# Kernel tuning notes

Measured on AMD Instinct MI355X. Metric: run time of the kernel, lower is better.

The kernel has to match this reference:

```python
import jax, jax.numpy as jnp
import numpy as np

N_NODES = 50000
N_EDGES = 600000
NFEAT = 128
HIDDEN = 64
NCLASS = 40


def sage_conv(x, src, dst, Wl, bl, Wr, num_nodes):
    # PyG SAGEConv (aggr='mean'): out = lin_l(mean_{j->i} x_j) + lin_r(x_i)
    msg = x[src]                                                  # [E, d]
    agg = jax.ops.segment_sum(msg, dst, num_segments=num_nodes)   # [N, d]
    cnt = jax.ops.segment_sum(jnp.ones((src.shape[0],), x.dtype), dst,
                              num_segments=num_nodes)             # [N]
    agg = agg / jnp.maximum(cnt, 1.0)[:, None]
    return agg @ Wl.T + bl + x @ Wr.T


def setup_inputs() -> dict:
    key = jax.random.key(0)
    ks = jax.random.split(key, 8)
    x = jax.random.normal(ks[0], (N_NODES, NFEAT), dtype=jnp.float32)
    edge_index = jax.random.randint(ks[1], (2, N_EDGES), 0, N_NODES, dtype=jnp.int64)
    def glorot(k, shape):
        lim = np.sqrt(6.0 / (shape[0] + shape[1]))
        return jax.random.uniform(k, shape, jnp.float32, -lim, lim)
    Wl1 = glorot(ks[2], (HIDDEN, NFEAT))
    bl1 = jnp.zeros((HIDDEN,), jnp.float32)
    Wr1 = glorot(ks[3], (HIDDEN, NFEAT))
    Wl2 = glorot(ks[4], (NCLASS, HIDDEN))
    bl2 = jnp.zeros((NCLASS,), jnp.float32)
    Wr2 = glorot(ks[5], (NCLASS, HIDDEN))
    return {"x": x, "edge_index": edge_index, "Wl1": Wl1, "bl1": bl1,
            "Wr1": Wr1, "Wl2": Wl2, "bl2": bl2, "Wr2": Wr2}


def reference(x, edge_index, Wl1, bl1, Wr1, Wl2, bl2, Wr2):
    src, dst = edge_index[0], edge_index[1]
    h = sage_conv(x, src, dst, Wl1, bl1, Wr1, N_NODES)   # [N, 64]
    h = jax.nn.sigmoid(h)
    out = sage_conv(h, src, dst, Wl2, bl2, Wr2, N_NODES)  # [N, nclass]
    return out
```

## Files before the change

kernel.cpp:

```cpp
#include <hip/hip_runtime.h>
#include <cmath>

#define NN 50000
#define NE 600000
#define NF 128
#define NH 64
#define NC 40

#define SCAN_TPB 512
#define SCAN_NBLK 98

#define LDSP1 65
#define LDSP2 41

__global__ __launch_bounds__(256) void k_hist(const int* __restrict__ dst,
                                              int* __restrict__ deg) {
  int i0 = blockIdx.x * blockDim.x + threadIdx.x;
  int stride = gridDim.x * blockDim.x;
  for (int e = i0; e < NE; e += stride) atomicAdd(&deg[dst[e]], 1);
}

__global__ __launch_bounds__(SCAN_TPB) void k_scan1(const int* __restrict__ deg,
                                                    int* __restrict__ blocksum) {
  __shared__ int sd[SCAN_TPB];
  int i = blockIdx.x * SCAN_TPB + threadIdx.x;
  sd[threadIdx.x] = (i < NN) ? deg[i] : 0;
  __syncthreads();
  for (int off = SCAN_TPB / 2; off > 0; off >>= 1) {
    if (threadIdx.x < off) sd[threadIdx.x] += sd[threadIdx.x + off];
    __syncthreads();
  }
  if (threadIdx.x == 0) blocksum[blockIdx.x] = sd[0];
}

__global__ __launch_bounds__(128) void k_scan2(const int* __restrict__ blocksum,
                                               int* __restrict__ blockoff) {
  __shared__ int sd[128];
  int tid = threadIdx.x;
  int v = (tid < SCAN_NBLK) ? blocksum[tid] : 0;
  sd[tid] = v;
  __syncthreads();
  for (int off = 1; off < 128; off <<= 1) {
    int t = (tid >= off) ? sd[tid - off] : 0;
    __syncthreads();
    sd[tid] += t;
    __syncthreads();
  }
  if (tid < SCAN_NBLK) blockoff[tid] = sd[tid] - v;
}

__global__ __launch_bounds__(SCAN_TPB) void k_scan3(
    const int* __restrict__ deg, const int* __restrict__ blockoff,
    int* __restrict__ rowptr, int* __restrict__ cursor) {
  __shared__ int sd[SCAN_TPB];
  int tid = threadIdx.x;
  int i = blockIdx.x * SCAN_TPB + tid;
  int v = (i < NN) ? deg[i] : 0;
  sd[tid] = v;
  __syncthreads();
  for (int off = 1; off < SCAN_TPB; off <<= 1) {
    int t = (tid >= off) ? sd[tid - off] : 0;
    __syncthreads();
    sd[tid] += t;
    __syncthreads();
  }
  if (i < NN) {
    int excl = blockoff[blockIdx.x] + sd[tid] - v;
    rowptr[i] = excl;
    cursor[i] = excl;
  }
}

__global__ __launch_bounds__(256) void k_fill(const int* __restrict__ src,
                                              const int* __restrict__ dst,
                                              int* __restrict__ cursor,
                                              int* __restrict__ eid) {
  int i0 = blockIdx.x * blockDim.x + threadIdx.x;
  int stride = gridDim.x * blockDim.x;
  for (int e = i0; e < NE; e += stride) {
    int pos = atomicAdd(&cursor[dst[e]], 1);
    eid[pos] = src[e];
  }
}

__global__ __launch_bounds__(512, 4) void k_dual_proj1(
    const float* __restrict__ X, const float* __restrict__ Wl,
    const float* __restrict__ Wr, const float* __restrict__ bl,
    float* __restrict__ P, float* __restrict__ Q) {
  __shared__ float swl[NF * LDSP1];
  __shared__ float swr[NF * LDSP1];
  int tid = threadIdx.x;
  for (int i = tid; i < NF * NH; i += 512) {
    int o = i >> 7, k = i & 127;
    swl[k * LDSP1 + o] = Wl[i];
    swr[k * LDSP1 + o] = Wr[i];
  }
  __syncthreads();
  int lane = tid & 63;
  int wave = blockIdx.x * 8 + (tid >> 6);
  int nw = gridDim.x * 8;
  float blv = bl[lane];
  const int ngroups = NN / 4;
  for (int g = wave; g < ngroups; g += nw) {
    int n0 = g * 4;
    const float4* xr = (const float4*)(X + (size_t)n0 * NF);
    float accP[4], accQ[4];
#pragma unroll
    for (int m = 0; m < 4; ++m) { accP[m] = 0.f; accQ[m] = 0.f; }
#pragma unroll 4
    for (int kk = 0; kk < 32; ++kk) {
      const float* wl4 = &swl[(kk * 4) * LDSP1 + lane];
      const float* wr4 = &swr[(kk * 4) * LDSP1 + lane];
      float l0 = wl4[0], l1 = wl4[LDSP1], l2 = wl4[2 * LDSP1], l3 = wl4[3 * LDSP1];
      float r0 = wr4[0], r1 = wr4[LDSP1], r2 = wr4[2 * LDSP1], r3 = wr4[3 * LDSP1];
#pragma unroll
      for (int m = 0; m < 4; ++m) {
        float4 v = xr[m * 32 + kk];
        accP[m] += v.x * l0 + v.y * l1 + v.z * l2 + v.w * l3;
        accQ[m] += v.x * r0 + v.y * r1 + v.z * r2 + v.w * r3;
      }
    }
#pragma unroll
    for (int m = 0; m < 4; ++m) {
      P[(size_t)(n0 + m) * NH + lane] = accP[m];
      Q[(size_t)(n0 + m) * NH + lane] = accQ[m] + blv;
    }
  }
}

__global__ __launch_bounds__(256) void k_dual_proj2(
    const float* __restrict__ H, const float* __restrict__ Wl,
    const float* __restrict__ Wr, const float* __restrict__ bl,
    float* __restrict__ P2, float* __restrict__ Q2) {
  __shared__ float swl[NH * LDSP2 + 64];
  __shared__ float swr[NH * LDSP2 + 64];
  int tid = threadIdx.x;
  for (int i = tid; i < NC * NH; i += 256) {
    int j = i >> 6, k = i & 63;
    swl[k * LDSP2 + j] = Wl[i];
    swr[k * LDSP2 + j] = Wr[i];
  }
  __syncthreads();
  int lane = tid & 63;
  int wave = blockIdx.x * 4 + (tid >> 6);
  int nw = gridDim.x * 4;
  float blv = (lane < NC) ? bl[lane] : 0.f;
  const int ngroups = NN / 8;
  for (int g = wave; g < ngroups; g += nw) {
    int n0 = g * 8;
    const float4* hr = (const float4*)(H + (size_t)n0 * NH);
    float accP[8], accQ[8];
#pragma unroll
    for (int m = 0; m < 8; ++m) { accP[m] = 0.f; accQ[m] = 0.f; }
#pragma unroll 4
    for (int kk = 0; kk < 16; ++kk) {
      const float* wl4 = &swl[(kk * 4) * LDSP2 + lane];
      const float* wr4 = &swr[(kk * 4) * LDSP2 + lane];
      float l0 = wl4[0], l1 = wl4[LDSP2], l2 = wl4[2 * LDSP2], l3 = wl4[3 * LDSP2];
      float r0 = wr4[0], r1 = wr4[LDSP2], r2 = wr4[2 * LDSP2], r3 = wr4[3 * LDSP2];
#pragma unroll
      for (int m = 0; m < 8; ++m) {
        float4 v = hr[m * 16 + kk];
        accP[m] += v.x * l0 + v.y * l1 + v.z * l2 + v.w * l3;
        accQ[m] += v.x * r0 + v.y * r1 + v.z * r2 + v.w * r3;
      }
    }
    if (lane < NC) {
#pragma unroll
      for (int m = 0; m < 8; ++m) {
        P2[(size_t)(n0 + m) * NC + lane] = accP[m];
        Q2[(size_t)(n0 + m) * NC + lane] = accQ[m] + blv;
      }
    }
  }
}

__global__ __launch_bounds__(256) void k_gather64(
    const float* __restrict__ P, const float* __restrict__ Q,
    const int* __restrict__ rowptr, const int* __restrict__ deg,
    const int* __restrict__ eid, float* __restrict__ H) {
  int lane = threadIdx.x & 63;
  int h = lane >> 5, c2 = lane & 31;
  int wave = blockIdx.x * 4 + (threadIdx.x >> 6);
  int nw = gridDim.x * 4;
  for (int n = wave; n < NN; n += nw) {
    int r0 = rowptr[n], dg = deg[n];
    float ax0 = 0.f, ay0 = 0.f, ax1 = 0.f, ay1 = 0.f;
    for (int base = 0; base < dg; base += 64) {
      int e = dg - base;
      if (e > 64) e = 64;
      int myeid = (lane < e) ? eid[r0 + base + lane] : 0;
      int j = 0;
      for (; j + 8 <= e; j += 8) {
        int sA = __shfl(myeid, j + h);
        int sB = __shfl(myeid, j + 2 + h);
        int sC = __shfl(myeid, j + 4 + h);
        int sD = __shfl(myeid, j + 6 + h);
        float2 vA = *(const float2*)(P + (size_t)sA * NH + 2 * c2);
        float2 vB = *(const float2*)(P + (size_t)sB * NH + 2 * c2);
        float2 vC = *(const float2*)(P + (size_t)sC * NH + 2 * c2);
        float2 vD = *(const float2*)(P + (size_t)sD * NH + 2 * c2);
        ax0 += vA.x + vC.x; ay0 += vA.y + vC.y;
        ax1 += vB.x + vD.x; ay1 += vB.y + vD.y;
      }
      for (; j + 4 <= e; j += 4) {
        int sA = __shfl(myeid, j + h);
        int sB = __shfl(myeid, j + 2 + h);
        float2 vA = *(const float2*)(P + (size_t)sA * NH + 2 * c2);
        float2 vB = *(const float2*)(P + (size_t)sB * NH + 2 * c2);
        ax0 += vA.x; ay0 += vA.y;
        ax1 += vB.x; ay1 += vB.y;
      }
      for (; j < e; j += 2) {
        int sA = __shfl(myeid, j + h);
        if (j + h < e) {
          float2 vA = *(const float2*)(P + (size_t)sA * NH + 2 * c2);
          ax0 += vA.x; ay0 += vA.y;
        }
      }
    }
    float sx = ax0 + ax1, sy = ay0 + ay1;
    sx += __shfl_xor(sx, 32);
    sy += __shfl_xor(sy, 32);
    if (h == 0) {
      float inv = 1.0f / (float)(dg > 0 ? dg : 1);
      float2 qv = *(const float2*)(Q + (size_t)n * NH + 2 * c2);
      float vx = sx * inv + qv.x;
      float vy = sy * inv + qv.y;
      float2 o;
      o.x = 1.0f / (1.0f + __expf(-vx));
      o.y = 1.0f / (1.0f + __expf(-vy));
      *(float2*)(H + (size_t)n * NH + 2 * c2) = o;
    }
  }
}

__global__ __launch_bounds__(256) void k_gather40(
    const float* __restrict__ P2, const float* __restrict__ Q2,
    const int* __restrict__ rowptr, const int* __restrict__ deg,
    const int* __restrict__ eid, float* __restrict__ Out) {
  int lane = threadIdx.x & 63;
  int h = lane >> 5, c2 = lane & 31;
  int wave = blockIdx.x * 4 + (threadIdx.x >> 6);
  int nw = gridDim.x * 4;
  for (int n = wave; n < NN; n += nw) {
    int r0 = rowptr[n], dg = deg[n];
    float ax0 = 0.f, ay0 = 0.f, ax1 = 0.f, ay1 = 0.f;
    for (int base = 0; base < dg; base += 64) {
      int e = dg - base;
      if (e > 64) e = 64;
      int myeid = (lane < e) ? eid[r0 + base + lane] : 0;
      int j = 0;
      for (; j + 8 <= e; j += 8) {
        int sA = __shfl(myeid, j + h);
        int sB = __shfl(myeid, j + 2 + h);
        int sC = __shfl(myeid, j + 4 + h);
        int sD = __shfl(myeid, j + 6 + h);
        if (c2 < 20) {
          float2 vA = *(const float2*)(P2 + (size_t)sA * NC + 2 * c2);
          float2 vB = *(const float2*)(P2 + (size_t)sB * NC + 2 * c2);
          float2 vC = *(const float2*)(P2 + (size_t)sC * NC + 2 * c2);
          float2 vD = *(const float2*)(P2 + (size_t)sD * NC + 2 * c2);
          ax0 += vA.x + vC.x; ay0 += vA.y + vC.y;
          ax1 += vB.x + vD.x; ay1 += vB.y + vD.y;
        }
      }
      for (; j + 4 <= e; j += 4) {
        int sA = __shfl(myeid, j + h);
        int sB = __shfl(myeid, j + 2 + h);
        if (c2 < 20) {
          float2 vA = *(const float2*)(P2 + (size_t)sA * NC + 2 * c2);
          float2 vB = *(const float2*)(P2 + (size_t)sB * NC + 2 * c2);
          ax0 += vA.x; ay0 += vA.y;
          ax1 += vB.x; ay1 += vB.y;
        }
      }
      for (; j < e; j += 2) {
        int sA = __shfl(myeid, j + h);
        if (c2 < 20 && (j + h) < e) {
          float2 vA = *(const float2*)(P2 + (size_t)sA * NC + 2 * c2);
          ax0 += vA.x; ay0 += vA.y;
        }
      }
    }
    float sx = ax0 + ax1, sy = ay0 + ay1;
    sx += __shfl_xor(sx, 32);
    sy += __shfl_xor(sy, 32);
    if (h == 0 && c2 < 20) {
      float inv = 1.0f / (float)(dg > 0 ? dg : 1);
      float2 qv = *(const float2*)(Q2 + (size_t)n * NC + 2 * c2);
      float2 o;
      o.x = sx * inv + qv.x;
      o.y = sy * inv + qv.y;
      *(float2*)(Out + (size_t)n * NC + 2 * c2) = o;
    }
  }
}

extern "C" void kernel_launch(void* const* d_in, const int* in_sizes, int n_in,
                              void* d_out, int out_size, void* d_ws,
                              size_t ws_size, hipStream_t stream) {
  const float* x = (const float*)d_in[0];
  const int* ei = (const int*)d_in[1];
  const float* Wl1 = (const float*)d_in[2];
  const float* bl1 = (const float*)d_in[3];
  const float* Wr1 = (const float*)d_in[4];
  const float* Wl2 = (const float*)d_in[5];
  const float* bl2 = (const float*)d_in[6];
  const float* Wr2 = (const float*)d_in[7];
  float* out = (float*)d_out;

  const int* src = ei;
  const int* dst = ei + NE;

  float* fws = (float*)d_ws;
  float* p1 = fws;
  float* q1 = p1 + (size_t)NN * NH;
  float* h = q1 + (size_t)NN * NH;
  float* p2 = fws;
  float* q2 = fws + (size_t)NN * NC;
  int* deg = (int*)(h + (size_t)NN * NH);
  int* rowptr = deg + NN;
  int* cursor = rowptr + NN;
  int* blocksum = cursor + NN;
  int* blockoff = blocksum + 128;
  int* eid = blockoff + 128;

  hipMemsetAsync(deg, 0, NN * sizeof(int), stream);

  k_hist<<<1024, 256, 0, stream>>>(dst, deg);
  k_scan1<<<SCAN_NBLK, SCAN_TPB, 0, stream>>>(deg, blocksum);
  k_scan2<<<1, 128, 0, stream>>>(blocksum, blockoff);
  k_scan3<<<SCAN_NBLK, SCAN_TPB, 0, stream>>>(deg, blockoff, rowptr, cursor);
  k_fill<<<1024, 256, 0, stream>>>(src, dst, cursor, eid);

  k_dual_proj1<<<512, 512, 0, stream>>>(x, Wl1, Wr1, bl1, p1, q1);
  k_gather64<<<2048, 256, 0, stream>>>(p1, q1, rowptr, deg, eid, h);

  k_dual_proj2<<<1024, 256, 0, stream>>>(h, Wl2, Wr2, bl2, p2, q2);
  k_gather40<<<2048, 256, 0, stream>>>(p2, q2, rowptr, deg, eid, out);
}
```

Baseline: 307.3 us.

## Store projected neighbor features in bf16 to halve gather traffic

The neighbor-side projections P and P2 are now written as bf16 (round-to-nearest-even) and unpacked to fp32 inside the gather kernels. This halves the bytes fetched per edge in the random-access aggregation, which is the memory-bound part. The first projection also processes 8 nodes per wave instead of 4, and both projection grids are resized. The price is reduced precision in the aggregated messages, which may push results toward the accuracy tolerance.

After: 364.4 us. +18.6%, slower.

```diff
diff --git a/kernel.cpp b/kernel.cpp
--- a/kernel.cpp
+++ b/kernel.cpp
@@ -12,6 +12,15 @@
 
 #define LDSP1 65
 #define LDSP2 41
+
+typedef unsigned int uint32;
+typedef unsigned short ushort16;
+
+static __device__ __forceinline__ ushort16 f2bf(float f) {
+  uint32 u = __float_as_uint(f);
+  uint32 r = 0x7fffu + ((u >> 16) & 1u);
+  return (ushort16)((u + r) >> 16);
+}
 
 __global__ __launch_bounds__(256) void k_hist(const int* __restrict__ dst,
                                               int* __restrict__ deg) {
@@ -86,7 +95,7 @@
 __global__ __launch_bounds__(512, 4) void k_dual_proj1(
     const float* __restrict__ X, const float* __restrict__ Wl,
     const float* __restrict__ Wr, const float* __restrict__ bl,
-    float* __restrict__ P, float* __restrict__ Q) {
+    ushort16* __restrict__ Pb, float* __restrict__ Q) {
   __shared__ float swl[NF * LDSP1];
   __shared__ float swr[NF * LDSP1];
   int tid = threadIdx.x;
@@ -100,13 +109,13 @@
   int wave = blockIdx.x * 8 + (tid >> 6);
   int nw = gridDim.x * 8;
   float blv = bl[lane];
-  const int ngroups = NN / 4;
+  const int ngroups = NN / 8;
   for (int g = wave; g < ngroups; g += nw) {
-    int n0 = g * 4;
+    int n0 = g * 8;
     const float4* xr = (const float4*)(X + (size_t)n0 * NF);
-    float accP[4], accQ[4];
-#pragma unroll
-    for (int m = 0; m < 4; ++m) { accP[m] = 0.f; accQ[m] = 0.f; }
+    float accP[8], accQ[8];
+#pragma unroll
+    for (int m = 0; m < 8; ++m) { accP[m] = 0.f; accQ[m] = 0.f; }
 #pragma unroll 4
     for (int kk = 0; kk < 32; ++kk) {
       const float* wl4 = &swl[(kk * 4) * LDSP1 + lane];
@@ -114,15 +123,15 @@
       float l0 = wl4[0], l1 = wl4[LDSP1], l2 = wl4[2 * LDSP1], l3 = wl4[3 * LDSP1];
       float r0 = wr4[0], r1 = wr4[LDSP1], r2 = wr4[2 * LDSP1], r3 = wr4[3 * LDSP1];
 #pragma unroll
-      for (int m = 0; m < 4; ++m) {
+      for (int m = 0; m < 8; ++m) {
         float4 v = xr[m * 32 + kk];
         accP[m] += v.x * l0 + v.y * l1 + v.z * l2 + v.w * l3;
         accQ[m] += v.x * r0 + v.y * r1 + v.z * r2 + v.w * r3;
       }
     }
 #pragma unroll
-    for (int m = 0; m < 4; ++m) {
-      P[(size_t)(n0 + m) * NH + lane] = accP[m];
+    for (int m = 0; m < 8; ++m) {
+      Pb[(size_t)(n0 + m) * NH + lane] = f2bf(accP[m]);
       Q[(size_t)(n0 + m) * NH + lane] = accQ[m] + blv;
     }
   }
@@ -131,7 +140,7 @@
 __global__ __launch_bounds__(256) void k_dual_proj2(
     const float* __restrict__ H, const float* __restrict__ Wl,
     const float* __restrict__ Wr, const float* __restrict__ bl,
-    float* __restrict__ P2, float* __restrict__ Q2) {
+    ushort16* __restrict__ P2b, float* __restrict__ Q2) {
   __shared__ float swl[NH * LDSP2 + 64];
   __shared__ float swr[NH * LDSP2 + 64];
   int tid = threadIdx.x;
@@ -168,7 +177,7 @@
     if (lane < NC) {
 #pragma unroll
       for (int m = 0; m < 8; ++m) {
-        P2[(size_t)(n0 + m) * NC + lane] = accP[m];
+        P2b[(size_t)(n0 + m) * NC + lane] = f2bf(accP[m]);
         Q2[(size_t)(n0 + m) * NC + lane] = accQ[m] + blv;
       }
     }
@@ -176,7 +185,7 @@
 }
 
 __global__ __launch_bounds__(256) void k_gather64(
-    const float* __restrict__ P, const float* __restrict__ Q,
+    const ushort16* __restrict__ Pb, const float* __restrict__ Q,
     const int* __restrict__ rowptr, const int* __restrict__ deg,
     const int* __restrict__ eid, float* __restrict__ H) {
   int lane = threadIdx.x & 63;
@@ -196,26 +205,31 @@
         int sB = __shfl(myeid, j + 2 + h);
         int sC = __shfl(myeid, j + 4 + h);
         int sD = __shfl(myeid, j + 6 + h);
-        float2 vA = *(const float2*)(P + (size_t)sA * NH + 2 * c2);
-        float2 vB = *(const float2*)(P + (size_t)sB * NH + 2 * c2);
-        float2 vC = *(const float2*)(P + (size_t)sC * NH + 2 * c2);
-        float2 vD = *(const float2*)(P + (size_t)sD * NH + 2 * c2);
-        ax0 += vA.x + vC.x; ay0 += vA.y + vC.y;
-        ax1 += vB.x + vD.x; ay1 += vB.y + vD.y;
+        uint32 uA = *(const uint32*)(Pb + (size_t)sA * NH + 2 * c2);
+        uint32 uB = *(const uint32*)(Pb + (size_t)sB * NH + 2 * c2);
+        uint32 uC = *(const uint32*)(Pb + (size_t)sC * NH + 2 * c2);
+        uint32 uD = *(const uint32*)(Pb + (size_t)sD * NH + 2 * c2);
+        ax0 += __uint_as_float(uA << 16) + __uint_as_float(uC << 16);
+        ay0 += __uint_as_float(uA & 0xffff0000u) + __uint_as_float(uC & 0xffff0000u);
+        ax1 += __uint_as_float(uB << 16) + __uint_as_float(uD << 16);
+        ay1 += __uint_as_float(uB & 0xffff0000u) + __uint_as_float(uD & 0xffff0000u);
       }
       for (; j + 4 <= e; j += 4) {
         int sA = __shfl(myeid, j + h);
         int sB = __shfl(myeid, j + 2 + h);
-        float2 vA = *(const float2*)(P + (size_t)sA * NH + 2 * c2);
-        float2 vB = *(const float2*)(P + (size_t)sB * NH + 2 * c2);
-        ax0 += vA.x; ay0 += vA.y;
-        ax1 += vB.x; ay1 += vB.y;
+        uint32 uA = *(const uint32*)(Pb + (size_t)sA * NH + 2 * c2);
+        uint32 uB = *(const uint32*)(Pb + (size_t)sB * NH + 2 * c2);
+        ax0 += __uint_as_float(uA << 16);
+        ay0 += __uint_as_float(uA & 0xffff0000u);
+        ax1 += __uint_as_float(uB << 16);
+        ay1 += __uint_as_float(uB & 0xffff0000u);
       }
       for (; j < e; j += 2) {
         int sA = __shfl(myeid, j + h);
         if (j + h < e) {
-          float2 vA = *(const float2*)(P + (size_t)sA * NH + 2 * c2);
-          ax0 += vA.x; ay0 += vA.y;
+          uint32 uA = *(const uint32*)(Pb + (size_t)sA * NH + 2 * c2);
+          ax0 += __uint_as_float(uA << 16);
+          ay0 += __uint_as_float(uA & 0xffff0000u);
         }
       }
     }
@@ -236,7 +250,7 @@
 }
 
 __global__ __launch_bounds__(256) void k_gather40(
-    const float* __restrict__ P2, const float* __restrict__ Q2,
+    const ushort16* __restrict__ P2b, const float* __restrict__ Q2,
     const int* __restrict__ rowptr, const int* __restrict__ deg,
     const int* __restrict__ eid, float* __restrict__ Out) {
   int lane = threadIdx.x & 63;
@@ -257,29 +271,34 @@
         int sC = __shfl(myeid, j + 4 + h);
         int sD = __shfl(myeid, j + 6 + h);
         if (c2 < 20) {
-          float2 vA = *(const float2*)(P2 + (size_t)sA * NC + 2 * c2);
-          float2 vB = *(const float2*)(P2 + (size_t)sB * NC + 2 * c2);
-          float2 vC = *(const float2*)(P2 + (size_t)sC * NC + 2 * c2);
-          float2 vD = *(const float2*)(P2 + (size_t)sD * NC + 2 * c2);
-          ax0 += vA.x + vC.x; ay0 += vA.y + vC.y;
-          ax1 += vB.x + vD.x; ay1 += vB.y + vD.y;
+          uint32 uA = *(const uint32*)(P2b + (size_t)sA * NC + 2 * c2);
+          uint32 uB = *(const uint32*)(P2b + (size_t)sB * NC + 2 * c2);
+          uint32 uC = *(const uint32*)(P2b + (size_t)sC * NC + 2 * c2);
+          uint32 uD = *(const uint32*)(P2b + (size_t)sD * NC + 2 * c2);
+          ax0 += __uint_as_float(uA << 16) + __uint_as_float(uC << 16);
+          ay0 += __uint_as_float(uA & 0xffff0000u) + __uint_as_float(uC & 0xffff0000u);
+          ax1 += __uint_as_float(uB << 16) + __uint_as_float(uD << 16);
+          ay1 += __uint_as_float(uB & 0xffff0000u) + __uint_as_float(uD & 0xffff0000u);
         }
       }
       for (; j + 4 <= e; j += 4) {
         int sA = __shfl(myeid, j + h);
         int sB = __shfl(myeid, j + 2 + h);
         if (c2 < 20) {
-          float2 vA = *(const float2*)(P2 + (size_t)sA * NC + 2 * c2);
-          float2 vB = *(const float2*)(P2 + (size_t)sB * NC + 2 * c2);
-          ax0 += vA.x; ay0 += vA.y;
-          ax1 += vB.x; ay1 += vB.y;
+          uint32 uA = *(const uint32*)(P2b + (size_t)sA * NC + 2 * c2);
+          uint32 uB = *(const uint32*)(P2b + (size_t)sB * NC + 2 * c2);
+          ax0 += __uint_as_float(uA << 16);
+          ay0 += __uint_as_float(uA & 0xffff0000u);
+          ax1 += __uint_as_float(uB << 16);
+          ay1 += __uint_as_float(uB & 0xffff0000u);
         }
       }
       for (; j < e; j += 2) {
         int sA = __shfl(myeid, j + h);
         if (c2 < 20 && (j + h) < e) {
-          float2 vA = *(const float2*)(P2 + (size_t)sA * NC + 2 * c2);
-          ax0 += vA.x; ay0 += vA.y;
+          uint32 uA = *(const uint32*)(P2b + (size_t)sA * NC + 2 * c2);
+          ax0 += __uint_as_float(uA << 16);
+          ay0 += __uint_as_float(uA & 0xffff0000u);
         }
       }
     }
@@ -313,13 +332,13 @@
   const int* src = ei;
   const int* dst = ei + NE;
 
-  float* fws = (float*)d_ws;
-  float* p1 = fws;
-  float* q1 = p1 + (size_t)NN * NH;
+  char* ws = (char*)d_ws;
+  ushort16* p1b = (ushort16*)ws;
+  float* q1 = (float*)(ws + (size_t)NN * NH * 2);
   float* h = q1 + (size_t)NN * NH;
-  float* p2 = fws;
-  float* q2 = fws + (size_t)NN * NC;
-  int* deg = (int*)(h + (size_t)NN * NH);
+  float* q2 = h + (size_t)NN * NH;
+  ushort16* p2b = (ushort16*)(q2 + (size_t)NN * NC);
+  int* deg = (int*)((char*)p2b + (size_t)NN * NC * 2);
   int* rowptr = deg + NN;
   int* cursor = rowptr + NN;
   int* blocksum = cursor + NN;
@@ -334,9 +353,9 @@
   k_scan3<<<SCAN_NBLK, SCAN_TPB, 0, stream>>>(deg, blockoff, rowptr, cursor);
   k_fill<<<1024, 256, 0, stream>>>(src, dst, cursor, eid);
 
-  k_dual_proj1<<<512, 512, 0, stream>>>(x, Wl1, Wr1, bl1, p1, q1);
-  k_gather64<<<2048, 256, 0, stream>>>(p1, q1, rowptr, deg, eid, h);
-
-  k_dual_proj2<<<1024, 256, 0, stream>>>(h, Wl2, Wr2, bl2, p2, q2);
-  k_gather40<<<2048, 256, 0, stream>>>(p2, q2, rowptr, deg, eid, out);
-}
+  k_dual_proj1<<<782, 512, 0, stream>>>(x, Wl1, Wr1, bl1, p1b, q1);
+  k_gather64<<<2048, 256, 0, stream>>>(p1b, q1, rowptr, deg, eid, h);
+
+  k_dual_proj2<<<1563, 256, 0, stream>>>(h, Wl2, Wr2, bl2, p2b, q2);
+  k_gather40<<<2048, 256, 0, stream>>>(p2b, q2, rowptr, deg, eid, out);
+}
```
